# Performance work log

Hardware: AMD Instinct MI355X
Metric: run time of the kernel (lower is better)

Reference implementation:

```python
import jax, jax.numpy as jnp
import numpy as np

B, T, D, H, K, ED = 4, 1024, 512, 8, 30, 128
HD = D // H
SCALE = HD ** -0.5


def _ln(x, g, b, eps=1e-5):
    m = jnp.mean(x, axis=-1, keepdims=True)
    v = jnp.var(x, axis=-1, keepdims=True)
    return (x - m) / jnp.sqrt(v + eps) * g + b


def setup_inputs() -> dict:
    key = jax.random.key(0)
    ks = jax.random.split(key, 16)
    s = 0.02
    return {
        "h_V": jax.random.normal(ks[0], (B, T, D), jnp.float32),
        "k": jax.random.normal(ks[1], (B, T, D), jnp.float32),
        "v": jax.random.normal(ks[2], (B, T, D), jnp.float32),
        "E": jax.random.normal(ks[3], (B, T, K, ED), jnp.float32),
        "bias": jax.random.normal(ks[4], (B, T, T), jnp.float32),
        "Wq": jax.random.normal(ks[5], (D, D), jnp.float32) * s,
        "bq": jnp.zeros((D,), jnp.float32),
        "Wk": jax.random.normal(ks[6], (D, D), jnp.float32) * s,
        "bk": jnp.zeros((D,), jnp.float32),
        "Wv": jax.random.normal(ks[7], (D, D), jnp.float32) * s,
        "bv": jnp.zeros((D,), jnp.float32),
        "Wo": jax.random.normal(ks[8], (D, D + ED), jnp.float32) * s,
        "bo": jnp.zeros((D,), jnp.float32),
        "t": jax.random.normal(ks[9], (1,), jnp.float32),
        "gn": jnp.ones((D,), jnp.float32),
        "bn": jnp.zeros((D,), jnp.float32),
        "w1": jax.random.normal(ks[10], (4 * D, D), jnp.float32) * s,
        "bw1": jnp.zeros((4 * D,), jnp.float32),
        "w2": jax.random.normal(ks[11], (D, 4 * D), jnp.float32) * s,
        "bw2": jnp.zeros((D,), jnp.float32),
        "gf": jnp.ones((D,), jnp.float32),
        "bf": jnp.zeros((D,), jnp.float32),
        "g2": jnp.ones((D,), jnp.float32),
        "b2": jnp.zeros((D,), jnp.float32),
        "E_idx": jax.random.randint(ks[12], (B, T, K), 0, T),
        "mask": jax.random.randint(ks[13], (B, T), 0, 2).astype(jnp.int32),
    }


def reference(h_V, k, v, E, bias, Wq, bq, Wk, bk, Wv, bv, Wo, bo, t, gn, bn, w1, bw1, w2, bw2, gf, bf, g2, b2, E_idx, mask):
    # q/k/v projections; q scaled by head_dim**-0.5 (as in torch: q *= scaling)
    q = (h_V @ Wq.T + bq) * SCALE
    kk = k @ Wk.T + bk
    vv = v @ Wv.T + bv
    qh = q.reshape(B, T, H, HD)
    kh = kk.reshape(B, T, H, HD)
    vh = vv.reshape(B, T, H, HD)
    # attention logits with additive pairwise bias, broadcast over heads
    aw = jnp.einsum('bthd,bshd->bhts', qh, kh) + bias[:, None, :, :]
    aw = jnp.where(mask[:, None, None, :] == 0, -1e9, aw)
    # h_attend temperature scaling
    aw = aw / (4.0 ** jnp.tanh(t[0]))
    p = jax.nn.softmax(aw, axis=-1)  # [B,H,T,S]
    attn = jnp.einsum('bhts,bshd->bthd', p, vh).reshape(B, T, D)
    # edge path: head-mean attention, gather neighbor weights, weighted edge sum
    ma = jnp.mean(p, axis=1)                       # [B,T,S]
    g = jnp.take_along_axis(ma, E_idx, axis=-1)    # [B,T,K]
    edge = (g[..., None] * E).sum(axis=2) / (g.sum(axis=-1, keepdims=True) + 1e-6)  # [B,T,ED]
    out = jnp.concatenate([attn, edge], axis=-1) @ Wo.T + bo
    h = _ln(h_V + out, gn, bn, eps=1e-5)
    # PositionwiseFeedForward: residual + LN(eps=1e-6)
    ff = jax.nn.gelu(h @ w1.T + bw1, approximate=False) @ w2.T + bw2
    dh = _ln(h + ff, gf, bf, eps=1e-6)
    return _ln(h + dh, g2, b2, eps=1e-5)
```

## Files before the change

kernel.cpp:

```cpp
#include <hip/hip_runtime.h>
#include <hip/hip_fp16.h>
#include <math.h>

#define B_ 4
#define T_ 1024
#define D_ 512
#define H_ 8
#define HD_ 64
#define KN 30
#define ED_ 128
#define DFF_ 2048
#define M_ 4096
#define BH_ 32

typedef _Float16 f16;
typedef __attribute__((ext_vector_type(8))) _Float16 f16x8;
typedef __attribute__((ext_vector_type(4))) _Float16 f16x4;
typedef __attribute__((ext_vector_type(4))) float f32x4;

#define MFMA16 __builtin_amdgcn_mfma_f32_16x16x32_f16
#define LOG2E 1.44269504088896f

__device__ __forceinline__ f16x8 ld8(const f16* p){ return *reinterpret_cast<const f16x8*>(p); }

__device__ __forceinline__ void gld16(const void* g, void* l){
  __builtin_amdgcn_global_load_lds((const __attribute__((address_space(1))) void*)g,
                                   (__attribute__((address_space(3))) void*)l, 16, 0, 0);
}

struct CvtJobs {
  const float* s[9];
  f16* d[9];
  int start[10];
};

__global__ __launch_bounds__(256) void cvt9_kernel(CvtJobs J){
  const int blk = blockIdx.x;
  int j = 0;
  while (j < 8 && blk >= J.start[j+1]) ++j;
  const int i = (blk - J.start[j])*256 + threadIdx.x;
  float4 v = reinterpret_cast<const float4*>(J.s[j])[i];
  union { f16 h[4]; ushort4 u; } o;
  o.h[0]=(f16)v.x; o.h[1]=(f16)v.y; o.h[2]=(f16)v.z; o.h[3]=(f16)v.w;
  reinterpret_cast<ushort4*>(J.d[j])[i] = o.u;
}

__global__ __launch_bounds__(256) void biasprep_kernel(
    const float* __restrict__ bias, const int* __restrict__ mask,
    const float* __restrict__ tsc, f16* __restrict__ biasP)
{
  const int gid = blockIdx.x*256 + threadIdx.x;
  const float s = exp2f(-2.0f*tanhf(tsc[0]))*LOG2E;
  const int b = gid >> 17;
  const int rem = gid & 131071;
  const int idx8 = rem*8;
  const int s0 = idx8 & 1023;
  const size_t gbase = (size_t)b*T_*T_ + idx8;
  float4 v0 = *reinterpret_cast<const float4*>(bias + gbase);
  float4 v1 = *reinterpret_cast<const float4*>(bias + gbase + 4);
  int4 m0 = *reinterpret_cast<const int4*>(mask + b*T_ + s0);
  int4 m1 = *reinterpret_cast<const int4*>(mask + b*T_ + s0 + 4);
  float x[8] = {v0.x,v0.y,v0.z,v0.w,v1.x,v1.y,v1.z,v1.w};
  int  mm[8] = {m0.x,m0.y,m0.z,m0.w,m1.x,m1.y,m1.z,m1.w};
  union { f16 h[8]; ushort4 u[2]; } o;
#pragma unroll
  for (int i = 0; i < 8; ++i){
    float t = (x[i] + (mm[i] ? 0.f : -60000.f))*s;
    o.h[i] = (f16)fmaxf(t, -60000.f);
  }
  reinterpret_cast<ushort4*>(biasP + gbase)[0] = o.u[0];
  reinterpret_cast<ushort4*>(biasP + gbase)[1] = o.u[1];
}

template<int EPI>
__global__ __launch_bounds__(256,2) void gemm_tile(
    const f16* __restrict__ X, const f16* __restrict__ W,
    const float* __restrict__ bias, void* __restrict__ outp,
    int Kd, int ldo, int nbN)
{
  __shared__ f16 As[128*64];
  __shared__ f16 Bs[128*64];
  const int nwg = gridDim.x;
  const int bid = blockIdx.x;
  const int swz = (bid & 7)*(nwg >> 3) + (bid >> 3);
  const int mb = swz / nbN, nb = swz - mb*nbN;
  const int rb = mb*128, cb = nb*128;
  const int tid = threadIdx.x;
  const int w = tid >> 6, lane = tid & 63;
  const int l16 = lane & 15, l4 = lane >> 4;
  const int wr = w >> 1, wc = w & 1;
  const int key = l16 & 7;

  f32x4 acc[4][4];
#pragma unroll
  for (int m = 0; m < 4; ++m)
#pragma unroll
    for (int n = 0; n < 4; ++n) acc[m][n] = (f32x4){0.f,0.f,0.f,0.f};

  for (int k0 = 0; k0 < Kd; k0 += 64){
#pragma unroll
    for (int i = 0; i < 4; ++i){
      const int cidx = i*256 + w*64 + lane;
      const int r = cidx >> 3, p = cidx & 7;
      gld16(X + (size_t)(rb + r)*Kd + k0 + ((p ^ (r & 7)) << 3),
            &As[(i*256 + w*64)*8]);
      gld16(W + (size_t)(cb + r)*Kd + k0 + ((p ^ (r & 7)) << 3),
            &Bs[(i*256 + w*64)*8]);
    }
    __syncthreads();
#pragma unroll
    for (int kk = 0; kk < 2; ++kk){
      f16x8 a[4], b[4];
#pragma unroll
      for (int m = 0; m < 4; ++m)
        a[m] = ld8(&As[(wr*64 + m*16 + l16)*64 + (((kk*4 + l4) ^ key) << 3)]);
#pragma unroll
      for (int n = 0; n < 4; ++n)
        b[n] = ld8(&Bs[(wc*64 + n*16 + l16)*64 + (((kk*4 + l4) ^ key) << 3)]);
#pragma unroll
      for (int m = 0; m < 4; ++m)
#pragma unroll
        for (int n = 0; n < 4; ++n)
          acc[m][n] = MFMA16(a[m], b[n], acc[m][n], 0,0,0);
    }
    __syncthreads();
  }

#pragma unroll
  for (int n = 0; n < 4; ++n){
    const int col = cb + wc*64 + n*16 + l16;
    const float bv = bias[col];
#pragma unroll
    for (int m = 0; m < 4; ++m){
#pragma unroll
      for (int j = 0; j < 4; ++j){
        const int row = rb + wr*64 + m*16 + l4*4 + j;
        float v = acc[m][n][j] + bv;
        if (EPI == 1){
          v = 0.5f*v*(1.0f + erff(v*0.70710678118654752f));
          ((f16*)outp)[(size_t)row*ldo + col] = (f16)v;
        } else {
          ((float*)outp)[(size_t)row*ldo + col] = v;
        }
      }
    }
  }
}

template<int EPI>
__global__ __launch_bounds__(256,2) void gemm_n64(
    const f16* __restrict__ X, const f16* __restrict__ W,
    const float* __restrict__ bias, void* __restrict__ outp,
    int Kd, int ldo, int nbN)
{
  __shared__ f16 As[128*64];
  __shared__ f16 Bs[64*64];
  const int nwg = gridDim.x;
  const int bid = blockIdx.x;
  const int swz = (bid & 7)*(nwg >> 3) + (bid >> 3);
  const int mb = swz / nbN, nb = swz - mb*nbN;
  const int rb = mb*128, cb = nb*64;
  const int tid = threadIdx.x;
  const int w = tid >> 6, lane = tid & 63;
  const int l16 = lane & 15, l4 = lane >> 4;
  const int wr = w >> 1, wc = w & 1;
  const int key = l16 & 7;

  f32x4 acc[4][2];
#pragma unroll
  for (int m = 0; m < 4; ++m)
#pragma unroll
    for (int n = 0; n < 2; ++n) acc[m][n] = (f32x4){0.f,0.f,0.f,0.f};

  for (int k0 = 0; k0 < Kd; k0 += 64){
#pragma unroll
    for (int i = 0; i < 4; ++i){
      const int cidx = i*256 + w*64 + lane;
      const int r = cidx >> 3, p = cidx & 7;
      gld16(X + (size_t)(rb + r)*Kd + k0 + ((p ^ (r & 7)) << 3),
            &As[(i*256 + w*64)*8]);
    }
#pragma unroll
    for (int i = 0; i < 2; ++i){
      const int cidx = i*256 + w*64 + lane;
      const int r = cidx >> 3, p = cidx & 7;
      gld16(W + (size_t)(cb + r)*Kd + k0 + ((p ^ (r & 7)) << 3),
            &Bs[(i*256 + w*64)*8]);
    }
    __syncthreads();
#pragma unroll
    for (int kk = 0; kk < 2; ++kk){
      f16x8 a[4], b[2];
#pragma unroll
      for (int m = 0; m < 4; ++m)
        a[m] = ld8(&As[(wr*64 + m*16 + l16)*64 + (((kk*4 + l4) ^ key) << 3)]);
#pragma unroll
      for (int n = 0; n < 2; ++n)
        b[n] = ld8(&Bs[(wc*32 + n*16 + l16)*64 + (((kk*4 + l4) ^ key) << 3)]);
#pragma unroll
      for (int m = 0; m < 4; ++m)
#pragma unroll
        for (int n = 0; n < 2; ++n)
          acc[m][n] = MFMA16(a[m], b[n], acc[m][n], 0,0,0);
    }
    __syncthreads();
  }

#pragma unroll
  for (int n = 0; n < 2; ++n){
    const int col = cb + wc*32 + n*16 + l16;
    const float bv = bias[col];
#pragma unroll
    for (int m = 0; m < 4; ++m){
#pragma unroll
      for (int j = 0; j < 4; ++j){
        const int row = rb + wr*64 + m*16 + l4*4 + j;
        float v = acc[m][n][j] + bv;
        if (EPI == 1){
          v = 0.5f*v*(1.0f + erff(v*0.70710678118654752f));
          ((f16*)outp)[(size_t)row*ldo + col] = (f16)v;
        } else {
          ((float*)outp)[(size_t)row*ldo + col] = v;
        }
      }
    }
  }
}

__global__ __launch_bounds__(256,2) void qkv_tile(
    const f16* __restrict__ hV, const f16* __restrict__ kI, const f16* __restrict__ vI,
    const f16* __restrict__ Wq, const f16* __restrict__ Wk, const f16* __restrict__ Wv,
    const float* __restrict__ bq, const float* __restrict__ bk, const float* __restrict__ bv,
    const float* __restrict__ tsc,
    f16* __restrict__ qo, f16* __restrict__ ko, f16* __restrict__ vT)
{
  __shared__ f16 As[128*32];
  __shared__ f16 Bs[128*32];
  const int bid = blockIdx.x;
  const int swz = (bid & 7)*48 + (bid >> 3);
  const int g = swz >> 7;
  const int r = swz & 127;
  const int mb = r >> 2, nb = r & 3;
  const f16* X  = (g == 0) ? hV : ((g == 1) ? kI : vI);
  const f16* W  = (g == 0) ? Wq : ((g == 1) ? Wk : Wv);
  const float* bias = (g == 0) ? bq : ((g == 1) ? bk : bv);
  const int rb = mb*128, cb = nb*128;
  const int tid = threadIdx.x;
  const int w = tid >> 6, lane = tid & 63;
  const int l16 = lane & 15, l4 = lane >> 4;
  const int wr = w >> 1, wc = w & 1;
  const int sr = lane >> 2, sc = (lane & 3)*8;
  const f16* Ax0 = X + (size_t)(rb + w*16 + sr)*D_ + sc;
  const f16* Ax1 = X + (size_t)(rb + 64 + w*16 + sr)*D_ + sc;
  const f16* Bx0 = W + (size_t)(cb + w*16 + sr)*D_ + sc;
  const f16* Bx1 = W + (size_t)(cb + 64 + w*16 + sr)*D_ + sc;
  f16* Ad0 = &As[(w*16)*32];
  f16* Ad1 = &As[(64 + w*16)*32];
  f16* Bd0 = &Bs[(w*16)*32];
  f16* Bd1 = &Bs[(64 + w*16)*32];

  f32x4 acc[4][4];
#pragma unroll
  for (int m = 0; m < 4; ++m)
#pragma unroll
    for (int n = 0; n < 4; ++n) acc[m][n] = (f32x4){0.f,0.f,0.f,0.f};

  for (int k0 = 0; k0 < D_; k0 += 32){
    gld16(Ax0 + k0, Ad0);
    gld16(Ax1 + k0, Ad1);
    gld16(Bx0 + k0, Bd0);
    gld16(Bx1 + k0, Bd1);
    __syncthreads();
    f16x8 a[4], b[4];
#pragma unroll
    for (int m = 0; m < 4; ++m) a[m] = ld8(&As[(wr*64 + m*16 + l16)*32 + l4*8]);
#pragma unroll
    for (int n = 0; n < 4; ++n) b[n] = ld8(&Bs[(wc*64 + n*16 + l16)*32 + l4*8]);
#pragma unroll
    for (int m = 0; m < 4; ++m)
#pragma unroll
      for (int n = 0; n < 4; ++n)
        acc[m][n] = MFMA16(a[m], b[n], acc[m][n], 0,0,0);
    __syncthreads();
  }

  const float qs = exp2f(-2.0f*tanhf(tsc[0]))*LOG2E*0.125f;
  const float scale = (g == 0) ? qs : 1.0f;
  f16* out = (g == 0) ? qo : ko;
#pragma unroll
  for (int n = 0; n < 4; ++n){
    const int col = cb + wc*64 + n*16 + l16;
    const float bv = bias[col];
#pragma unroll
    for (int m = 0; m < 4; ++m){
#pragma unroll
      for (int j = 0; j < 4; ++j){
        const int row = rb + wr*64 + m*16 + l4*4 + j;
        const float v = (acc[m][n][j] + bv)*scale;
        if (g < 2){
          out[(size_t)row*D_ + col] = (f16)v;
        } else {
          const int b = row >> 10, t = row & (T_-1);
          const int h = col >> 6,  dl = col & (HD_-1);
          vT[(((size_t)b*H_ + h)*HD_ + dl)*T_ + t] = (f16)v;
        }
      }
    }
  }
}

__global__ __launch_bounds__(512,4) void attn_fused(
    const f16* __restrict__ q, const f16* __restrict__ k, const f16* __restrict__ vT,
    const f16* __restrict__ biasP, const int* __restrict__ eidx,
    f16* __restrict__ X2, float* __restrict__ gpart)
{
  __shared__ f16 Sb[8192];
  __shared__ f16 Pc[32*128];
  __shared__ float red[2][2][4][16];
  const int bid = blockIdx.x;
  const int swz = (bid & 7)*128 + (bid >> 3);
  const int bh = swz >> 5, tb = swz & 31;
  const int bi = bh >> 3, h = bh & 7;
  const int t0 = tb*32;
  const int tid = threadIdx.x, w = tid >> 6, lane = tid & 63;
  const int qg = w >> 2, ws = w & 3;
  const int l16 = lane & 15, l4 = lane >> 4;
  const int key = l16 & 7;

  const f16* qp = q + (size_t)(bi*T_ + t0 + qg*16 + l16)*D_ + h*HD_ + l4*8;
  const f16x8 q0 = ld8(qp), q1 = ld8(qp + 32);
  int g_id0, g_r0, g_kk0, g_id1 = -1, g_r1 = 0, g_kk1 = 0;
  g_r0 = tid/KN; g_kk0 = tid - g_r0*KN;
  g_id0 = eidx[((size_t)(bi*T_ + t0 + g_r0))*KN + g_kk0];
  if (tid + 512 < 32*KN){
    g_r1 = (tid+512)/KN; g_kk1 = (tid+512) - g_r1*KN;
    g_id1 = eidx[((size_t)(bi*T_ + t0 + g_r1))*KN + g_kk1];
  }

  const f16* kg = k + (size_t)(bi*T_)*D_ + h*HD_;
  const f16* bg = biasP + ((size_t)(bi*T_ + t0))*T_;
  const f16* vg = vT + (size_t)bh*HD_*T_;

  f32x4 acc[16];
#pragma unroll
  for (int c = 0; c < 8; ++c){
    if (c) __syncthreads();
#pragma unroll
    for (int i = 0; i < 2; ++i){
      const int cidx = i*512 + w*64 + lane;
      const int r = cidx >> 3, p = cidx & 7;
      gld16(kg + (size_t)(c*128 + r)*D_ + ((p ^ (r & 7)) << 3),
            &Sb[(i*512 + w*64)*8]);
    }
    {
      const int cidx = w*64 + lane;
      const int r = cidx >> 4, p = cidx & 15;
      gld16(bg + (size_t)r*T_ + c*128 + ((p ^ (r & 7)) << 3),
            &Pc[(w*64)*8]);
    }
    __syncthreads();
#pragma unroll
    for (int step = 0; step < 2; ++step){
      const int r = ws*32 + step*16 + l16;
      f32x4 a = {0.f,0.f,0.f,0.f};
      a = MFMA16(ld8(&Sb[r*64 + ((l4 ^ key) << 3)]),       q0, a, 0,0,0);
      a = MFMA16(ld8(&Sb[r*64 + (((4 + l4) ^ key) << 3)]), q1, a, 0,0,0);
      const int slb = ws*32 + step*16 + l4*4;
      const f16x4 bf = *reinterpret_cast<const f16x4*>(
          &Pc[(qg*16 + l16)*128 + (((slb >> 3) ^ key) << 3) + (slb & 7)]);
#pragma unroll
      for (int j = 0; j < 4; ++j) a[j] += (float)bf[j];
      acc[c*2 + step] = a;
    }
  }

  float m = -3.4e38f;
#pragma unroll
  for (int c = 0; c < 16; ++c)
#pragma unroll
    for (int j = 0; j < 4; ++j) m = fmaxf(m, acc[c][j]);
  m = fmaxf(m, __shfl_xor(m, 16));
  m = fmaxf(m, __shfl_xor(m, 32));
  if (lane < 16) red[0][qg][ws][lane] = m;
  __syncthreads();
  m = fmaxf(fmaxf(red[0][qg][0][l16], red[0][qg][1][l16]),
            fmaxf(red[0][qg][2][l16], red[0][qg][3][l16]));
  float l = 0.f;
#pragma unroll
  for (int c = 0; c < 16; ++c)
#pragma unroll
    for (int j = 0; j < 4; ++j){
      const float e = exp2f(acc[c][j] - m);
      l += e;
      acc[c][j] = e;
    }
  l += __shfl_xor(l, 16);
  l += __shfl_xor(l, 32);
  if (lane < 16) red[1][qg][ws][lane] = l;

  f32x4 oo0 = {0.f,0.f,0.f,0.f}, oo1 = oo0, oo2 = oo0, oo3 = oo0;
#pragma unroll
  for (int sc = 0; sc < 8; ++sc){
    __syncthreads();
#pragma unroll
    for (int step = 0; step < 2; ++step){
      const int slb = ws*32 + step*16 + l4*4;
      f16x4 pp;
#pragma unroll
      for (int j = 0; j < 4; ++j) pp[j] = (f16)acc[sc*2 + step][j];
      *reinterpret_cast<f16x4*>(
          &Pc[(qg*16 + l16)*128 + (((slb >> 3) ^ key) << 3) + (slb & 7)]) = pp;
    }
#pragma unroll
    for (int i = 0; i < 2; ++i){
      const int cidx = i*512 + w*64 + lane;
      const int r = cidx >> 4, p = cidx & 15;
      gld16(vg + (size_t)r*T_ + sc*128 + ((p ^ (r & 7)) << 3),
            &Sb[(i*512 + w*64)*8]);
    }
    __syncthreads();
    const int vrow = (ws*16 + l16)*128;
#pragma unroll
    for (int grp = 0; grp < 4; ++grp){
      const int ch = (grp*4 + l4) ^ key;
      const f16x8 pa = ld8(&Pc[(qg*16 + l16)*128 + (ch << 3)]);
      const f16x8 vb = ld8(&Sb[vrow + (ch << 3)]);
      if (grp == 0)      oo0 = MFMA16(pa, vb, oo0, 0,0,0);
      else if (grp == 1) oo1 = MFMA16(pa, vb, oo1, 0,0,0);
      else if (grp == 2) oo2 = MFMA16(pa, vb, oo2, 0,0,0);
      else               oo3 = MFMA16(pa, vb, oo3, 0,0,0);
    }
    if ((g_id0 >> 7) == sc){
      const int r = g_r0;
      const float lr = red[1][r >> 4][0][r & 15] + red[1][r >> 4][1][r & 15]
                     + red[1][r >> 4][2][r & 15] + red[1][r >> 4][3][r & 15];
      const int sl = g_id0 & 127;
      const float pv = (float)Pc[r*128 + ((((sl >> 3) ^ (r & 7)) << 3) | (sl & 7))];
      gpart[((size_t)bh*T_ + t0 + r)*KN + g_kk0] = pv/lr*0.125f;
    }
    if (g_id1 >= 0 && (g_id1 >> 7) == sc){
      const int r = g_r1;
      const float lr = red[1][r >> 4][0][r & 15] + red[1][r >> 4][1][r & 15]
                     + red[1][r >> 4][2][r & 15] + red[1][r >> 4][3][r & 15];
      const int sl = g_id1 & 127;
      const float pv = (float)Pc[r*128 + ((((sl >> 3) ^ (r & 7)) << 3) | (sl & 7))];
      gpart[((size_t)bh*T_ + t0 + r)*KN + g_kk1] = pv/lr*0.125f;
    }
  }
  const f32x4 o = (oo0 + oo1) + (oo2 + oo3);

#pragma unroll
  for (int j = 0; j < 4; ++j){
    const int row = l4*4 + j;
    const float lr = red[1][qg][0][row] + red[1][qg][1][row]
                   + red[1][qg][2][row] + red[1][qg][3][row];
    const int t = t0 + qg*16 + row;
    X2[((size_t)(bi*T_ + t))*640 + h*HD_ + ws*16 + l16] = (f16)(o[j]/lr);
  }
}

__global__ __launch_bounds__(128) void edge_kernel(
    const float* __restrict__ gpart, const float* __restrict__ E, f16* __restrict__ X2)
{
  __shared__ float gl[KN];
  __shared__ float ginv;
  const int bt = blockIdx.x;
  const int bi = bt >> 10, tt = bt & 1023;
  const int t = threadIdx.x;
  if (t < KN){
    float s = 0.f;
#pragma unroll
    for (int hh = 0; hh < H_; ++hh)
      s += gpart[((size_t)(bi*H_ + hh)*T_ + tt)*KN + t];
    gl[t] = s;
  }
  __syncthreads();
  if (t == 0){
    float s = 0.f;
#pragma unroll
    for (int i = 0; i < KN; ++i) s += gl[i];
    ginv = 1.0f/(s + 1e-6f);
  }
  __syncthreads();
  float acc = 0.f;
  const float* Ep = E + (size_t)bt*KN*ED_ + t;
#pragma unroll 5
  for (int kk = 0; kk < KN; ++kk) acc += gl[kk]*Ep[(size_t)kk*ED_];
  X2[(size_t)bt*640 + 512 + t] = (f16)(acc*ginv);
}

__device__ __forceinline__ float block_sum(float v, float* sbuf){
  for (int o = 32; o; o >>= 1) v += __shfl_down(v, o);
  __syncthreads();
  if ((threadIdx.x & 63) == 0) sbuf[threadIdx.x >> 6] = v;
  __syncthreads();
  return sbuf[0]+sbuf[1]+sbuf[2]+sbuf[3];
}

__global__ __launch_bounds__(256) void ln1_kernel(
    const float* __restrict__ hV, const float* __restrict__ hraw,
    const float* __restrict__ gn, const float* __restrict__ bn,
    float* __restrict__ hf, f16* __restrict__ hh)
{
  __shared__ float sbuf[4];
  const int r = blockIdx.x, t = threadIdx.x;
  const size_t base = (size_t)r*D_;
  float x0 = hV[base+t]     + hraw[base+t];
  float x1 = hV[base+t+256] + hraw[base+t+256];
  float s = block_sum(x0+x1, sbuf);
  const float mean = s*(1.f/512.f);
  float d0 = x0-mean, d1 = x1-mean;
  float vs = block_sum(d0*d0+d1*d1, sbuf);
  const float rstd = rsqrtf(vs*(1.f/512.f) + 1e-5f);
  float y0 = d0*rstd*gn[t]     + bn[t];
  float y1 = d1*rstd*gn[t+256] + bn[t+256];
  hf[base+t]     = y0;  hh[base+t]     = (f16)y0;
  hf[base+t+256] = y1;  hh[base+t+256] = (f16)y1;
}

__global__ __launch_bounds__(256) void final_kernel(
    const float* __restrict__ hf, const float* __restrict__ ffr,
    const float* __restrict__ gf, const float* __restrict__ bfv,
    const float* __restrict__ g2, const float* __restrict__ b2,
    float* __restrict__ out)
{
  __shared__ float sbuf[4];
  const int r = blockIdx.x, t = threadIdx.x;
  const size_t base = (size_t)r*D_;
  const float h0 = hf[base+t], h1 = hf[base+t+256];
  float x0 = h0 + ffr[base+t], x1 = h1 + ffr[base+t+256];
  float s = block_sum(x0+x1, sbuf);
  float mean = s*(1.f/512.f);
  float d0 = x0-mean, d1 = x1-mean;
  float vs = block_sum(d0*d0+d1*d1, sbuf);
  float rstd = rsqrtf(vs*(1.f/512.f) + 1e-6f);
  const float dh0 = d0*rstd*gf[t]     + bfv[t];
  const float dh1 = d1*rstd*gf[t+256] + bfv[t+256];
  const float y0 = h0 + dh0, y1 = h1 + dh1;
  s = block_sum(y0+y1, sbuf);
  mean = s*(1.f/512.f);
  d0 = y0-mean; d1 = y1-mean;
  vs = block_sum(d0*d0+d1*d1, sbuf);
  rstd = rsqrtf(vs*(1.f/512.f) + 1e-5f);
  out[base+t]     = d0*rstd*g2[t]     + b2[t];
  out[base+t+256] = d1*rstd*g2[t+256] + b2[t+256];
}

extern "C" void kernel_launch(void* const* d_in, const int* in_sizes, int n_in,
                              void* d_out, int out_size, void* d_ws, size_t ws_size,
                              hipStream_t stream)
{
  (void)in_sizes; (void)n_in; (void)out_size;
  const float* h_V  = (const float*)d_in[0];
  const float* kin  = (const float*)d_in[1];
  const float* vin  = (const float*)d_in[2];
  const float* E    = (const float*)d_in[3];
  const float* bias = (const float*)d_in[4];
  const float* Wq   = (const float*)d_in[5];
  const float* bq   = (const float*)d_in[6];
  const float* Wk   = (const float*)d_in[7];
  const float* bk   = (const float*)d_in[8];
  const float* Wv   = (const float*)d_in[9];
  const float* bv   = (const float*)d_in[10];
  const float* Wo   = (const float*)d_in[11];
  const float* bo   = (const float*)d_in[12];
  const float* tsc  = (const float*)d_in[13];
  const float* gn   = (const float*)d_in[14];
  const float* bn   = (const float*)d_in[15];
  const float* w1   = (const float*)d_in[16];
  const float* bw1  = (const float*)d_in[17];
  const float* w2   = (const float*)d_in[18];
  const float* bw2  = (const float*)d_in[19];
  const float* gf   = (const float*)d_in[20];
  const float* bfv  = (const float*)d_in[21];
  const float* g2   = (const float*)d_in[22];
  const float* b2   = (const float*)d_in[23];
  const int*   Eidx = (const int*)d_in[24];
  const int*   mask = (const int*)d_in[25];
  float* out = (float*)d_out;

  char* wsb = (char*)d_ws;
  size_t off = 0;
  auto alloc = [&](size_t bytes) -> void* {
    void* pp = wsb + off; off += (bytes + 255) & ~(size_t)255; return pp;
  };
  f16* hVb  = (f16*)alloc((size_t)M_*D_*2);
  f16* kbI  = (f16*)alloc((size_t)M_*D_*2);
  f16* vbI  = (f16*)alloc((size_t)M_*D_*2);
  f16* Wqb  = (f16*)alloc((size_t)D_*D_*2);
  f16* Wkb  = (f16*)alloc((size_t)D_*D_*2);
  f16* Wvb  = (f16*)alloc((size_t)D_*D_*2);
  f16* Wob  = (f16*)alloc((size_t)D_*(D_+ED_)*2);
  f16* w1b  = (f16*)alloc((size_t)DFF_*D_*2);
  f16* w2b  = (f16*)alloc((size_t)D_*DFF_*2);
  f16* qb   = (f16*)alloc((size_t)M_*D_*2);
  f16* kb   = (f16*)alloc((size_t)M_*D_*2);
  f16* vT   = (f16*)alloc((size_t)M_*D_*2);
  f16* biasP= (f16*)alloc((size_t)B_*T_*T_*2);
  f16* X2   = (f16*)alloc((size_t)M_*640*2);
  float* gpart = (float*)alloc((size_t)BH_*T_*KN*4);
  float* hraw = (float*)alloc((size_t)M_*D_*4);
  float* hf   = (float*)alloc((size_t)M_*D_*4);
  f16*   hh   = (f16*)alloc((size_t)M_*D_*2);
  f16*   ff1  = (f16*)alloc((size_t)M_*DFF_*2);
  if (ws_size < off) return;
  float* ffraw = hraw;

  {
    CvtJobs J;
    const float* srcs[9] = {h_V, kin, vin, Wq, Wk, Wv, Wo, w1, w2};
    f16* dsts[9] = {hVb, kbI, vbI, Wqb, Wkb, Wvb, Wob, w1b, w2b};
    const int n4s[9] = {M_*D_/4, M_*D_/4, M_*D_/4, D_*D_/4, D_*D_/4, D_*D_/4,
                        D_*(D_+ED_)/4, DFF_*D_/4, D_*DFF_/4};
    int cum = 0;
    for (int i = 0; i < 9; ++i){
      J.s[i] = srcs[i]; J.d[i] = dsts[i]; J.start[i] = cum;
      cum += n4s[i]/256;
    }
    J.start[9] = cum;
    cvt9_kernel<<<cum,256,0,stream>>>(J);
  }
  biasprep_kernel<<<B_*T_*T_/8/256,256,0,stream>>>(bias, mask, tsc, biasP);

  qkv_tile<<<384,256,0,stream>>>(hVb, kbI, vbI, Wqb, Wkb, Wvb, bq, bk, bv, tsc, qb, kb, vT);

  attn_fused<<<1024,512,0,stream>>>(qb, kb, vT, biasP, Eidx, X2, gpart);

  edge_kernel<<<M_,128,0,stream>>>(gpart, E, X2);

  gemm_n64<2><<<256,256,0,stream>>>(X2, Wob, bo, hraw, D_+ED_, D_, 8);
  ln1_kernel<<<M_,256,0,stream>>>(h_V, hraw, gn, bn, hf, hh);

  gemm_tile<1><<<512,256,0,stream>>>(hh, w1b, bw1, ff1, D_, DFF_, 16);
  gemm_n64<2><<<256,256,0,stream>>>(ff1, w2b, bw2, ffraw, DFF_, D_, 8);

  final_kernel<<<M_,256,0,stream>>>(hf, ffraw, gf, bfv, g2, b2, out);
}
```

Measured before the change: 170.0 us.

## Double-buffer K/V staging in attention and pre-tile bias into MFMA fragment layout

```diff
diff --git a/kernel.cpp b/kernel.cpp
--- a/kernel.cpp
+++ b/kernel.cpp
@@ -47,29 +47,33 @@
 
 __global__ __launch_bounds__(256) void biasprep_kernel(
     const float* __restrict__ bias, const int* __restrict__ mask,
-    const float* __restrict__ tsc, f16* __restrict__ biasP)
-{
-  const int gid = blockIdx.x*256 + threadIdx.x;
+    const float* __restrict__ tsc, f16* __restrict__ biasT)
+{
+  const int TT = blockIdx.x*256 + threadIdx.x;
+  const int G = TT >> 4, l16 = TT & 15;
+  const int qg = G & 1, step = (G >> 1) & 1, ws = (G >> 2) & 3;
+  const int c = (G >> 4) & 7, tb = (G >> 7) & 31, bi = G >> 12;
   const float s = exp2f(-2.0f*tanhf(tsc[0]))*LOG2E;
-  const int b = gid >> 17;
-  const int rem = gid & 131071;
-  const int idx8 = rem*8;
-  const int s0 = idx8 & 1023;
-  const size_t gbase = (size_t)b*T_*T_ + idx8;
-  float4 v0 = *reinterpret_cast<const float4*>(bias + gbase);
-  float4 v1 = *reinterpret_cast<const float4*>(bias + gbase + 4);
-  int4 m0 = *reinterpret_cast<const int4*>(mask + b*T_ + s0);
-  int4 m1 = *reinterpret_cast<const int4*>(mask + b*T_ + s0 + 4);
-  float x[8] = {v0.x,v0.y,v0.z,v0.w,v1.x,v1.y,v1.z,v1.w};
-  int  mm[8] = {m0.x,m0.y,m0.z,m0.w,m1.x,m1.y,m1.z,m1.w};
-  union { f16 h[8]; ushort4 u[2]; } o;
-#pragma unroll
-  for (int i = 0; i < 8; ++i){
-    float t = (x[i] + (mm[i] ? 0.f : -60000.f))*s;
-    o.h[i] = (f16)fmaxf(t, -60000.f);
-  }
-  reinterpret_cast<ushort4*>(biasP + gbase)[0] = o.u[0];
-  reinterpret_cast<ushort4*>(biasP + gbase)[1] = o.u[1];
+  const int t  = tb*32 + qg*16 + l16;
+  const int s0 = c*128 + ws*32 + step*16;
+  const float* bp = bias + ((size_t)bi*T_ + t)*T_ + s0;
+  const int*   mp = mask + bi*T_ + s0;
+  union { f16 h[16]; f16x8 v8[2]; } o;
+#pragma unroll
+  for (int i = 0; i < 16; i += 4){
+    float4 v = *reinterpret_cast<const float4*>(bp + i);
+    int4  mm = *reinterpret_cast<const int4*>(mp + i);
+    float x[4] = {v.x,v.y,v.z,v.w};
+    int  m4[4] = {mm.x,mm.y,mm.z,mm.w};
+#pragma unroll
+    for (int j = 0; j < 4; ++j){
+      float tv = (x[j] + (m4[j] ? 0.f : -60000.f))*s;
+      o.h[i+j] = (f16)fmaxf(tv, -60000.f);
+    }
+  }
+  f16* op = biasT + (size_t)G*256 + l16*16;
+  reinterpret_cast<f16x8*>(op)[0] = o.v8[0];
+  reinterpret_cast<f16x8*>(op)[1] = o.v8[1];
 }
 
 template<int EPI>
@@ -311,12 +315,11 @@
 
 __global__ __launch_bounds__(512,4) void attn_fused(
     const f16* __restrict__ q, const f16* __restrict__ k, const f16* __restrict__ vT,
-    const f16* __restrict__ biasP, const int* __restrict__ eidx,
+    const f16* __restrict__ biasT, const int* __restrict__ eidx,
     f16* __restrict__ X2, float* __restrict__ gpart)
 {
-  __shared__ f16 Sb[8192];
+  __shared__ f16 Sb[16384];
   __shared__ f16 Pc[32*128];
-  __shared__ float red[2][2][4][16];
   const int bid = blockIdx.x;
   const int swz = (bid & 7)*128 + (bid >> 3);
   const int bh = swz >> 5, tb = swz & 31;
@@ -329,51 +332,64 @@
 
   const f16* qp = q + (size_t)(bi*T_ + t0 + qg*16 + l16)*D_ + h*HD_ + l4*8;
   const f16x8 q0 = ld8(qp), q1 = ld8(qp + 32);
-  int g_id0, g_r0, g_kk0, g_id1 = -1, g_r1 = 0, g_kk1 = 0;
-  g_r0 = tid/KN; g_kk0 = tid - g_r0*KN;
-  g_id0 = eidx[((size_t)(bi*T_ + t0 + g_r0))*KN + g_kk0];
-  if (tid + 512 < 32*KN){
-    g_r1 = (tid+512)/KN; g_kk1 = (tid+512) - g_r1*KN;
-    g_id1 = eidx[((size_t)(bi*T_ + t0 + g_r1))*KN + g_kk1];
+  const int tl = tid & 255;
+  int ga_r, ga_kk, ga_id, gb_r = 0, gb_kk = 0, gb_id = -1;
+  ga_r = tl/KN; ga_kk = tl - ga_r*KN;
+  ga_id = eidx[((size_t)(bi*T_ + t0 + qg*16 + ga_r))*KN + ga_kk];
+  if (tl + 256 < 16*KN){
+    gb_r = (tl+256)/KN; gb_kk = (tl+256) - gb_r*KN;
+    gb_id = eidx[((size_t)(bi*T_ + t0 + qg*16 + gb_r))*KN + gb_kk];
   }
 
   const f16* kg = k + (size_t)(bi*T_)*D_ + h*HD_;
-  const f16* bg = biasP + ((size_t)(bi*T_ + t0))*T_;
   const f16* vg = vT + (size_t)bh*HD_*T_;
-
-  f32x4 acc[16];
-#pragma unroll
-  for (int c = 0; c < 8; ++c){
-    if (c) __syncthreads();
+  const f16* bb = biasT + (size_t)(bi*32 + tb)*32768 + ws*1024 + qg*256 + l16*16 + l4*4;
+
+  auto stageK = [&](int c, int slot){
 #pragma unroll
     for (int i = 0; i < 2; ++i){
       const int cidx = i*512 + w*64 + lane;
       const int r = cidx >> 3, p = cidx & 7;
       gld16(kg + (size_t)(c*128 + r)*D_ + ((p ^ (r & 7)) << 3),
-            &Sb[(i*512 + w*64)*8]);
-    }
-    {
-      const int cidx = w*64 + lane;
+            &Sb[slot*8192 + (i*512 + w*64)*8]);
+    }
+  };
+  auto stageV = [&](int sc, int slot){
+#pragma unroll
+    for (int i = 0; i < 2; ++i){
+      const int cidx = i*512 + w*64 + lane;
       const int r = cidx >> 4, p = cidx & 15;
-      gld16(bg + (size_t)r*T_ + c*128 + ((p ^ (r & 7)) << 3),
-            &Pc[(w*64)*8]);
-    }
-    __syncthreads();
+      gld16(vg + (size_t)r*T_ + sc*128 + ((p ^ (r & 7)) << 3),
+            &Sb[slot*8192 + (i*512 + w*64)*8]);
+    }
+  };
+
+  f32x4 acc[16];
+  stageK(0, 0);
+#pragma unroll
+  for (int c = 0; c < 8; ++c){
+    if (c < 7) stageK(c+1, (c+1)&1);
+    if (c < 7) asm volatile("s_waitcnt vmcnt(2)" ::: "memory");
+    else       asm volatile("s_waitcnt vmcnt(0)" ::: "memory");
+    __builtin_amdgcn_sched_barrier(0);
+    __builtin_amdgcn_s_barrier();
+    __builtin_amdgcn_sched_barrier(0);
+    const int base = (c&1)*8192;
 #pragma unroll
     for (int step = 0; step < 2; ++step){
-      const int r = ws*32 + step*16 + l16;
+      const int rr = ws*32 + step*16 + l16;
       f32x4 a = {0.f,0.f,0.f,0.f};
-      a = MFMA16(ld8(&Sb[r*64 + ((l4 ^ key) << 3)]),       q0, a, 0,0,0);
-      a = MFMA16(ld8(&Sb[r*64 + (((4 + l4) ^ key) << 3)]), q1, a, 0,0,0);
-      const int slb = ws*32 + step*16 + l4*4;
-      const f16x4 bf = *reinterpret_cast<const f16x4*>(
-          &Pc[(qg*16 + l16)*128 + (((slb >> 3) ^ key) << 3) + (slb & 7)]);
+      a = MFMA16(ld8(&Sb[base + rr*64 + ((l4 ^ key) << 3)]),       q0, a, 0,0,0);
+      a = MFMA16(ld8(&Sb[base + rr*64 + (((4 + l4) ^ key) << 3)]), q1, a, 0,0,0);
+      const f16x4 bf = *reinterpret_cast<const f16x4*>(bb + c*4096 + step*512);
 #pragma unroll
       for (int j = 0; j < 4; ++j) a[j] += (float)bf[j];
       acc[c*2 + step] = a;
     }
-  }
-
+    __builtin_amdgcn_s_barrier();
+  }
+
+  float* redf = (float*)Sb;
   float m = -3.4e38f;
 #pragma unroll
   for (int c = 0; c < 16; ++c)
@@ -381,10 +397,10 @@
     for (int j = 0; j < 4; ++j) m = fmaxf(m, acc[c][j]);
   m = fmaxf(m, __shfl_xor(m, 16));
   m = fmaxf(m, __shfl_xor(m, 32));
-  if (lane < 16) red[0][qg][ws][lane] = m;
+  if (lane < 16) redf[(qg*4 + ws)*16 + lane] = m;
   __syncthreads();
-  m = fmaxf(fmaxf(red[0][qg][0][l16], red[0][qg][1][l16]),
-            fmaxf(red[0][qg][2][l16], red[0][qg][3][l16]));
+  m = fmaxf(fmaxf(redf[(qg*4+0)*16 + l16], redf[(qg*4+1)*16 + l16]),
+            fmaxf(redf[(qg*4+2)*16 + l16], redf[(qg*4+3)*16 + l16]));
   float l = 0.f;
 #pragma unroll
   for (int c = 0; c < 16; ++c)
@@ -396,12 +412,18 @@
     }
   l += __shfl_xor(l, 16);
   l += __shfl_xor(l, 32);
-  if (lane < 16) red[1][qg][ws][lane] = l;
+  if (lane < 16) redf[128 + (qg*4 + ws)*16 + lane] = l;
+  __syncthreads();
+  const float lrq = redf[128 + (qg*4+0)*16 + l16] + redf[128 + (qg*4+1)*16 + l16]
+                  + redf[128 + (qg*4+2)*16 + l16] + redf[128 + (qg*4+3)*16 + l16];
+  __syncthreads();
+  const float lr_a = __shfl(lrq, ga_r);
+  const float lr_b = __shfl(lrq, gb_r);
 
   f32x4 oo0 = {0.f,0.f,0.f,0.f}, oo1 = oo0, oo2 = oo0, oo3 = oo0;
+  stageV(0, 0);
 #pragma unroll
   for (int sc = 0; sc < 8; ++sc){
-    __syncthreads();
 #pragma unroll
     for (int step = 0; step < 2; ++step){
       const int slb = ws*32 + step*16 + l4*4;
@@ -411,50 +433,44 @@
       *reinterpret_cast<f16x4*>(
           &Pc[(qg*16 + l16)*128 + (((slb >> 3) ^ key) << 3) + (slb & 7)]) = pp;
     }
-#pragma unroll
-    for (int i = 0; i < 2; ++i){
-      const int cidx = i*512 + w*64 + lane;
-      const int r = cidx >> 4, p = cidx & 15;
-      gld16(vg + (size_t)r*T_ + sc*128 + ((p ^ (r & 7)) << 3),
-            &Sb[(i*512 + w*64)*8]);
-    }
-    __syncthreads();
+    if (sc < 7) stageV(sc+1, (sc+1)&1);
+    if (sc < 7) asm volatile("s_waitcnt vmcnt(2) lgkmcnt(0)" ::: "memory");
+    else        asm volatile("s_waitcnt vmcnt(0) lgkmcnt(0)" ::: "memory");
+    __builtin_amdgcn_sched_barrier(0);
+    __builtin_amdgcn_s_barrier();
+    __builtin_amdgcn_sched_barrier(0);
+    const int base = (sc&1)*8192;
     const int vrow = (ws*16 + l16)*128;
 #pragma unroll
     for (int grp = 0; grp < 4; ++grp){
       const int ch = (grp*4 + l4) ^ key;
       const f16x8 pa = ld8(&Pc[(qg*16 + l16)*128 + (ch << 3)]);
-      const f16x8 vb = ld8(&Sb[vrow + (ch << 3)]);
+      const f16x8 vb = ld8(&Sb[base + vrow + (ch << 3)]);
       if (grp == 0)      oo0 = MFMA16(pa, vb, oo0, 0,0,0);
       else if (grp == 1) oo1 = MFMA16(pa, vb, oo1, 0,0,0);
       else if (grp == 2) oo2 = MFMA16(pa, vb, oo2, 0,0,0);
       else               oo3 = MFMA16(pa, vb, oo3, 0,0,0);
     }
-    if ((g_id0 >> 7) == sc){
-      const int r = g_r0;
-      const float lr = red[1][r >> 4][0][r & 15] + red[1][r >> 4][1][r & 15]
-                     + red[1][r >> 4][2][r & 15] + red[1][r >> 4][3][r & 15];
-      const int sl = g_id0 & 127;
+    if ((ga_id >> 7) == sc){
+      const int r = qg*16 + ga_r;
+      const int sl = ga_id & 127;
       const float pv = (float)Pc[r*128 + ((((sl >> 3) ^ (r & 7)) << 3) | (sl & 7))];
-      gpart[((size_t)bh*T_ + t0 + r)*KN + g_kk0] = pv/lr*0.125f;
-    }
-    if (g_id1 >= 0 && (g_id1 >> 7) == sc){
-      const int r = g_r1;
-      const float lr = red[1][r >> 4][0][r & 15] + red[1][r >> 4][1][r & 15]
-                     + red[1][r >> 4][2][r & 15] + red[1][r >> 4][3][r & 15];
-      const int sl = g_id1 & 127;
+      gpart[((size_t)bh*T_ + t0 + r)*KN + ga_kk] = pv/lr_a*0.125f;
+    }
+    if (gb_id >= 0 && (gb_id >> 7) == sc){
+      const int r = qg*16 + gb_r;
+      const int sl = gb_id & 127;
       const float pv = (float)Pc[r*128 + ((((sl >> 3) ^ (r & 7)) << 3) | (sl & 7))];
-      gpart[((size_t)bh*T_ + t0 + r)*KN + g_kk1] = pv/lr*0.125f;
-    }
+      gpart[((size_t)bh*T_ + t0 + r)*KN + gb_kk] = pv/lr_b*0.125f;
+    }
+    __builtin_amdgcn_s_barrier();
   }
   const f32x4 o = (oo0 + oo1) + (oo2 + oo3);
 
 #pragma unroll
   for (int j = 0; j < 4; ++j){
-    const int row = l4*4 + j;
-    const float lr = red[1][qg][0][row] + red[1][qg][1][row]
-                   + red[1][qg][2][row] + red[1][qg][3][row];
-    const int t = t0 + qg*16 + row;
+    const float lr = __shfl(lrq, l4*4 + j);
+    const int t = t0 + qg*16 + l4*4 + j;
     X2[((size_t)(bi*T_ + t))*640 + h*HD_ + ws*16 + l16] = (f16)(o[j]/lr);
   }
 }
@@ -596,7 +612,7 @@
   f16* qb   = (f16*)alloc((size_t)M_*D_*2);
   f16* kb   = (f16*)alloc((size_t)M_*D_*2);
   f16* vT   = (f16*)alloc((size_t)M_*D_*2);
-  f16* biasP= (f16*)alloc((size_t)B_*T_*T_*2);
+  f16* biasT= (f16*)alloc((size_t)B_*T_*T_*2);
   f16* X2   = (f16*)alloc((size_t)M_*640*2);
   float* gpart = (float*)alloc((size_t)BH_*T_*KN*4);
   float* hraw = (float*)alloc((size_t)M_*D_*4);
@@ -620,11 +636,11 @@
     J.start[9] = cum;
     cvt9_kernel<<<cum,256,0,stream>>>(J);
   }
-  biasprep_kernel<<<B_*T_*T_/8/256,256,0,stream>>>(bias, mask, tsc, biasP);
+  biasprep_kernel<<<1024,256,0,stream>>>(bias, mask, tsc, biasT);
 
   qkv_tile<<<384,256,0,stream>>>(hVb, kbI, vbI, Wqb, Wkb, Wvb, bq, bk, bv, tsc, qb, kb, vT);
 
-  attn_fused<<<1024,512,0,stream>>>(qb, kb, vT, biasP, Eidx, X2, gpart);
+  attn_fused<<<1024,512,0,stream>>>(qb, kb, vT, biasT, Eidx, X2, gpart);
 
   edge_kernel<<<M_,128,0,stream>>>(gpart, E, X2);
 
```

Result: no change. 168.1 us (-1.1%).
